# Performance work log

Hardware: AMD Instinct MI355X
Metric: run time of the kernel (lower is better)

The kernel has to match this reference:

```python
import jax, jax.numpy as jnp
import numpy as np

C_IN = 1024
C_INTER = 512  # in_channels // 2, canonical NONLocalBlock default
N_CLASSES = 13


def setup_inputs() -> dict:
    key = jax.random.key(0)
    ks = jax.random.split(key, 11)
    B, T, H, W = 16, 8, 14, 14
    s = 0.02
    return {
        "x": jax.random.normal(ks[0], (B, C_IN, T, H, W), dtype=jnp.float32),
        # 1x1x1 conv projections stored as [out, in] matrices + biases
        "g_w": jax.random.normal(ks[1], (C_INTER, C_IN), dtype=jnp.float32) * s,
        "g_b": jnp.zeros((C_INTER,), dtype=jnp.float32),
        "theta_w": jax.random.normal(ks[2], (C_INTER, C_IN), dtype=jnp.float32) * s,
        "theta_b": jnp.zeros((C_INTER,), dtype=jnp.float32),
        "phi_w": jax.random.normal(ks[3], (C_INTER, C_IN), dtype=jnp.float32) * s,
        "phi_b": jnp.zeros((C_INTER,), dtype=jnp.float32),
        "w_w": jax.random.normal(ks[4], (C_IN, C_INTER), dtype=jnp.float32) * s,
        "w_b": jnp.zeros((C_IN,), dtype=jnp.float32),
        "fc_w": jax.random.normal(ks[5], (N_CLASSES, C_IN), dtype=jnp.float32) * s,
        "fc_b": jnp.zeros((N_CLASSES,), dtype=jnp.float32),
    }


def reference(x, g_w, g_b, theta_w, theta_b, phi_w, phi_b, w_w, w_b, fc_w, fc_b):
    B, C, T, H, W = x.shape
    xf = x.reshape(B, C, -1)  # [B, C, N], N = T*H*W
    # 1x1x1 conv projections == channel matmuls
    g = jnp.einsum('oc,bcn->bno', g_w, xf) + g_b        # [B, N, 512]
    th = jnp.einsum('oc,bcn->bno', theta_w, xf) + theta_b  # [B, N, 512]
    ph = jnp.einsum('oc,bcn->bno', phi_w, xf) + phi_b      # [B, N, 512]
    # pairwise affinity (embedded Gaussian): [B, N, N]
    f = jnp.einsum('bnd,bmd->bnm', th, ph)
    attn = jax.nn.softmax(f, axis=-1)
    y = jnp.einsum('bnm,bmd->bnd', attn, g)             # [B, N, 512]
    wy = jnp.einsum('cd,bnd->bcn', w_w, y) + w_b[None, :, None]  # [B, C, N]
    z = wy.reshape(B, C, T, H, W) + x                    # residual
    pooled = z.mean(axis=(2, 3, 4))                      # adaptive avgpool (1,1,1)
    return pooled @ fc_w.T + fc_b                        # [B, 13]
```

## Files before the change

### kernel.cpp

```cpp
#include <hip/hip_runtime.h>
#include <hip/hip_bf16.h>


#define BATCH 16
#define CIN   1024
#define CINT  512
#define NSP   1568
#define NPAD  1664
#define NTIL  13
#define NCLS  13

using bf16 = __hip_bfloat16;
typedef __attribute__((ext_vector_type(8))) short short8;
typedef __attribute__((ext_vector_type(4))) float f32x4;

#define DEVI static __device__ __forceinline__

DEVI void gload16(const void* g, void* l) {
  __builtin_amdgcn_global_load_lds((const __attribute__((address_space(1))) void*)g,
                                   (__attribute__((address_space(3))) void*)l, 16, 0, 0);
}

DEVI float wave_sum(float v) {
#pragma unroll
  for (int m = 32; m; m >>= 1) v += __shfl_xor(v, m);
  return v;
}

DEVI short f2bf(float f) {
  union { __hip_bfloat16 h; short s; } u;
  u.h = __float2bfloat16(f);
  return u.s;
}

__global__ __launch_bounds__(256) void k_transpose(const float* __restrict__ x,
                                                   bf16* __restrict__ xt,
                                                   float* __restrict__ xbar) {
  __shared__ float t[128 * 37];
  const int b = blockIdx.z;
  const int n0 = blockIdx.x * 32;
  const int c0 = blockIdx.y * 128;
  const int tid = threadIdx.x;
  const int lane = tid & 63;
  const float* xb = x + (size_t)b * CIN * NSP;
  const bool pad = (n0 >= NSP);
#pragma unroll
  for (int it = 0; it < 4; ++it) {
    const int slot = it * 256 + tid;
    const int cr = slot >> 3;
    const int q = slot & 7;
    float4 v = {0.f, 0.f, 0.f, 0.f};
    if (!pad) v = *(const float4*)(xb + (size_t)(c0 + cr) * NSP + n0 + q * 4);
    t[cr * 37 + q * 4 + 0] = v.x;
    t[cr * 37 + q * 4 + 1] = v.y;
    t[cr * 37 + q * 4 + 2] = v.z;
    t[cr * 37 + q * 4 + 3] = v.w;
    float s = v.x + v.y + v.z + v.w;
    s += __shfl_xor(s, 1);
    s += __shfl_xor(s, 2);
    s += __shfl_xor(s, 4);
    if ((lane & 7) == 0 && !pad)
      atomicAdd(&xbar[b * CIN + c0 + cr], s * (1.0f / NSP));
  }
  __syncthreads();
  bf16* xo = xt + (size_t)b * NPAD * CIN;
#pragma unroll
  for (int it = 0; it < 2; ++it) {
    const int slot = it * 256 + tid;
    const int n = slot >> 4;
    const int seg = slot & 15;
    short8 o;
#pragma unroll
    for (int k = 0; k < 8; ++k) o[k] = f2bf(t[(seg * 8 + k) * 37 + n]);
    *(short8*)(xo + (size_t)(n0 + n) * CIN + c0 + seg * 8) = o;
  }
}

__global__ void k_wconv(const float* __restrict__ thw, const float* __restrict__ phw,
                        bf16* __restrict__ wb) {
  const int i4 = (blockIdx.x * 256 + threadIdx.x) * 4;
  const float* s = (i4 < 512 * 1024) ? (thw + i4) : (phw + (i4 - 512 * 1024));
  const float4 v = *(const float4*)s;
  wb[i4 + 0] = __float2bfloat16(v.x);
  wb[i4 + 1] = __float2bfloat16(v.y);
  wb[i4 + 2] = __float2bfloat16(v.z);
  wb[i4 + 3] = __float2bfloat16(v.w);
}

template <int LDK>
DEVI void gemm128_bt(const bf16* Ag, const bf16* Bg, bf16* lds,
                     f32x4 acc[4][4]) {
  const int tid = threadIdx.x;
  const int lane = tid & 63;
  const int w = tid >> 6;
  const int wr = (w >> 1) * 64;
  const int wc = (w & 1) * 64;
  const int kc_src8 = ((lane & 3) ^ ((lane >> 3) & 3)) * 8;
  const int kc_rd8 = (((lane >> 4) ^ ((lane >> 1) & 3))) * 8;
  constexpr int NT = LDK / 32;

  auto STAGE = [&](int buf, int ks) {
    bf16* lA = lds + buf * 8192;
    bf16* lB = lA + 4096;
#pragma unroll
    for (int it = 0; it < 2; ++it) {
      const int ch = w * 64 + it * 256 + lane;
      const int row = ch >> 2;
      const int lbase = (w * 64 + it * 256) * 8;
      gload16(Ag + (size_t)row * LDK + ks * 32 + kc_src8, lA + lbase);
      gload16(Bg + (size_t)row * LDK + ks * 32 + kc_src8, lB + lbase);
    }
  };
  auto COMPUTE = [&](int buf) {
    const bf16* lA = lds + buf * 8192;
    const bf16* lB = lA + 4096;
    short8 af[4], bfr[4];
#pragma unroll
    for (int i = 0; i < 4; ++i)
      af[i] = *(const short8*)(lA + (wr + i * 16 + (lane & 15)) * 32 + kc_rd8);
#pragma unroll
    for (int i = 0; i < 4; ++i)
      bfr[i] = *(const short8*)(lB + (wc + i * 16 + (lane & 15)) * 32 + kc_rd8);
#pragma unroll
    for (int m = 0; m < 4; ++m)
#pragma unroll
      for (int n = 0; n < 4; ++n)
        acc[m][n] = __builtin_amdgcn_mfma_f32_16x16x32_bf16(af[m], bfr[n], acc[m][n], 0, 0, 0);
  };

  STAGE(0, 0);
  __syncthreads();
  int ks = 0;
#pragma unroll 1
  while (ks < NT - 2) {
    STAGE(1, ks + 1);
    COMPUTE(0);
    __syncthreads();
    STAGE(0, ks + 2);
    COMPUTE(1);
    __syncthreads();
    ks += 2;
  }
  STAGE(1, NT - 1);
  COMPUTE(0);
  __syncthreads();
  COMPUTE(1);
}

__global__ __launch_bounds__(256) void k_proj(const bf16* __restrict__ xt,
                                              const bf16* __restrict__ wb,
                                              const float* __restrict__ thb,
                                              const float* __restrict__ phb,
                                              bf16* __restrict__ th,
                                              bf16* __restrict__ ph) {
  __shared__ bf16 smem[16384];
  const int id = blockIdx.x;
  const int rcls = id & 7;
  const int q = id >> 3;
  const int bm = (q >> 3) * 8 + rcls;
  const int bo = q & 7;

  f32x4 acc[4][4];
  const f32x4 z = {0.f, 0.f, 0.f, 0.f};
#pragma unroll
  for (int m = 0; m < 4; ++m)
#pragma unroll
    for (int n = 0; n < 4; ++n) acc[m][n] = z;

  gemm128_bt<CIN>(xt + (size_t)bm * 128 * CIN, wb + (size_t)bo * 128 * CIN,
                  smem, acc);

  const int tid = threadIdx.x;
  const int lane = tid & 63;
  const int w = tid >> 6;
  const int wc = (w & 1) * 64;
  const int hsel = w >> 1;
  const float* bias = (bo < 4) ? thb : phb;
  bf16* outb = (bo < 4) ? th : ph;
  const int obase = (bo & 3) * 128;
#pragma unroll
  for (int h = 0; h < 2; ++h) {
    __syncthreads();
    if (hsel == h) {
#pragma unroll
      for (int m = 0; m < 4; ++m)
#pragma unroll
        for (int n = 0; n < 4; ++n) {
          const int col_l = wc + n * 16 + (lane & 15);
          const float bv = bias[obase + col_l];
#pragma unroll
          for (int j = 0; j < 4; ++j) {
            const int lr = m * 16 + (lane >> 4) * 4 + j;
            smem[lr * 128 + (col_l ^ ((lr & 7) << 3))] =
                __float2bfloat16(acc[m][n][j] + bv);
          }
        }
    }
    __syncthreads();
#pragma unroll
    for (int it = 0; it < 4; ++it) {
      const int slot = it * 256 + tid;
      const int rr = slot >> 4;
      const int seg = slot & 15;
      const short8 v = *(const short8*)(smem + rr * 128 + ((seg ^ (rr & 7)) << 3));
      *(short8*)(outb + (size_t)(bm * 128 + h * 64 + rr) * CINT + obase + seg * 8) = v;
    }
  }
}

__global__ __launch_bounds__(256) void k_fgemm(const bf16* __restrict__ th,
                                               const bf16* __restrict__ ph,
                                               bf16* __restrict__ eb,
                                               float* __restrict__ psum) {
  __shared__ bf16 smem[16384];
  __shared__ float rsum2[2][128];
  const int id = blockIdx.x;
  const int rcls = id & 7;
  const int q = id >> 3;
  const int bloc = q / 169;
  const int t = q - bloc * 169;
  const int b = bloc * 8 + rcls;
  const int bm = t / 13;
  const int bn = t - bm * 13;

  f32x4 acc[4][4];
  const f32x4 z = {0.f, 0.f, 0.f, 0.f};
#pragma unroll
  for (int m = 0; m < 4; ++m)
#pragma unroll
    for (int n = 0; n < 4; ++n) acc[m][n] = z;

  gemm128_bt<CINT>(th + ((size_t)b * NPAD + bm * 128) * CINT,
                   ph + ((size_t)b * NPAD + bn * 128) * CINT,
                   smem, acc);

  const int tid = threadIdx.x;
  const int lane = tid & 63;
  const int w = tid >> 6;
  const int wc = (w & 1) * 64;
  const int hsel = w >> 1;
  bf16* ebb = eb + ((size_t)b * NPAD + bm * 128) * NPAD + bn * 128;
#pragma unroll
  for (int h = 0; h < 2; ++h) {
    __syncthreads();
    if (hsel == h) {
#pragma unroll
      for (int m = 0; m < 4; ++m)
#pragma unroll
        for (int j = 0; j < 4; ++j) {
          const int lr = m * 16 + (lane >> 4) * 4 + j;
          float ps = 0.f;
#pragma unroll
          for (int n = 0; n < 4; ++n) {
            const int col_l = wc + n * 16 + (lane & 15);
            const float ev = __expf(acc[m][n][j]);
            smem[lr * 128 + (col_l ^ ((lr & 7) << 3))] = __float2bfloat16(ev);
            if (bn * 128 + col_l < NSP) ps += ev;
          }
          ps += __shfl_xor(ps, 1);
          ps += __shfl_xor(ps, 2);
          ps += __shfl_xor(ps, 4);
          ps += __shfl_xor(ps, 8);
          if ((lane & 15) == 0) rsum2[w & 1][h * 64 + lr] = ps;
        }
    }
    __syncthreads();
#pragma unroll
    for (int it = 0; it < 4; ++it) {
      const int slot = it * 256 + tid;
      const int rr = slot >> 4;
      const int seg = slot & 15;
      const short8 v = *(const short8*)(smem + rr * 128 + ((seg ^ (rr & 7)) << 3));
      *(short8*)(ebb + (size_t)(h * 64 + rr) * NPAD + seg * 8) = v;
    }
  }
  if (tid < 128)
    psum[((size_t)b * NTIL + bn) * NPAD + bm * 128 + tid] =
        rsum2[0][tid] + rsum2[1][tid];
}

__global__ void k_recip(const float* __restrict__ psum, float* __restrict__ rinv) {
  const int id = blockIdx.x * 256 + threadIdx.x;
  const int b = id / NSP;
  const int n = id - b * NSP;
  float s = 0.f;
#pragma unroll
  for (int t = 0; t < NTIL; ++t) s += psum[((size_t)b * NTIL + t) * NPAD + n];
  rinv[id] = 1.0f / s;
}

__global__ void k_abar(const bf16* __restrict__ eb, const float* __restrict__ rinv,
                       float* __restrict__ abar) {
  const int m = blockIdx.x * 256 + threadIdx.x;
  const int b = blockIdx.z;
  const bool act = m < NSP;
  const bf16* fb = eb + (size_t)b * NPAD * NPAD;
  const int n0 = blockIdx.y * 196;
  float local = 0.f;
  for (int n = n0; n < n0 + 196; ++n) {
    const float iS = rinv[b * NSP + n];
    if (act) local += __bfloat162float(fb[(size_t)n * NPAD + m]) * iS;
  }
  if (act) atomicAdd(&abar[b * NSP + m], local * (1.0f / NSP));
}

__global__ void k_xg(const bf16* __restrict__ xt, const float* __restrict__ abar,
                     float* __restrict__ xg) {
  const int c = blockIdx.x * 256 + threadIdx.x;
  const int b = blockIdx.z;
  const bf16* xb = xt + (size_t)b * NPAD * CIN;
  const int n0 = blockIdx.y * 196;
  float s = 0.f;
  for (int n = n0; n < n0 + 196; ++n)
    s += __bfloat162float(xb[(size_t)n * CIN + c]) * abar[b * NSP + n];
  atomicAdd(&xg[b * CIN + c], s);
}

__global__ __launch_bounds__(64) void k_ybar(const float* __restrict__ gw,
                                             const float* __restrict__ gb,
                                             const float* __restrict__ xg,
                                             float* __restrict__ syb) {
  const int d = blockIdx.x;
  const int lane = threadIdx.x;
  const float4* wr = (const float4*)(gw + (size_t)d * CIN);
  float4 wv[4];
#pragma unroll
  for (int k = 0; k < 4; ++k) wv[k] = wr[k * 64 + lane];
  const float bv = gb[d];
#pragma unroll 1
  for (int b = 0; b < BATCH; ++b) {
    const float4* xr = (const float4*)(xg + (size_t)b * CIN);
    float s = 0.f;
#pragma unroll
    for (int k = 0; k < 4; ++k) {
      const float4 xv = xr[k * 64 + lane];
      s += wv[k].x * xv.x + wv[k].y * xv.y + wv[k].z * xv.z + wv[k].w * xv.w;
    }
    s = wave_sum(s);
    if (lane == 0) syb[b * CINT + d] = s + bv;
  }
}

__global__ __launch_bounds__(64) void k_spool(const float* __restrict__ ww,
                                              const float* __restrict__ wbias,
                                              const float* __restrict__ xbar,
                                              const float* __restrict__ syb,
                                              float* __restrict__ spool) {
  const int c = blockIdx.x;
  const int lane = threadIdx.x;
  const float4* wr = (const float4*)(ww + (size_t)c * CINT);
  float4 wv[2];
#pragma unroll
  for (int k = 0; k < 2; ++k) wv[k] = wr[k * 64 + lane];
  const float bv = wbias[c];
#pragma unroll 1
  for (int b = 0; b < BATCH; ++b) {
    const float4* yr = (const float4*)(syb + (size_t)b * CINT);
    float s = 0.f;
#pragma unroll
    for (int k = 0; k < 2; ++k) {
      const float4 yv = yr[k * 64 + lane];
      s += wv[k].x * yv.x + wv[k].y * yv.y + wv[k].z * yv.z + wv[k].w * yv.w;
    }
    s = wave_sum(s);
    if (lane == 0) spool[b * CIN + c] = s + bv + xbar[b * CIN + c];
  }
}

__global__ __launch_bounds__(64) void k_out(const float* __restrict__ spool,
                                            const float* __restrict__ fcw,
                                            const float* __restrict__ fcb,
                                            float* __restrict__ out) {
  const int b = blockIdx.x;
  const int lane = threadIdx.x;
  const float4* pr = (const float4*)(spool + (size_t)b * CIN);
  float4 pv[4];
#pragma unroll
  for (int k = 0; k < 4; ++k) pv[k] = pr[k * 64 + lane];
#pragma unroll 1
  for (int cls = 0; cls < NCLS; ++cls) {
    const float4* wr = (const float4*)(fcw + (size_t)cls * CIN);
    float s = 0.f;
#pragma unroll
    for (int k = 0; k < 4; ++k) {
      const float4 wv = wr[k * 64 + lane];
      s += wv.x * pv[k].x + wv.y * pv[k].y + wv.z * pv[k].z + wv.w * pv[k].w;
    }
    s = wave_sum(s);
    if (lane == 0) out[b * NCLS + cls] = s + fcb[cls];
  }
}

extern "C" void kernel_launch(void* const* d_in, const int* in_sizes, int n_in,
                              void* d_out, int out_size, void* d_ws, size_t ws_size,
                              hipStream_t stream) {
  const float* x    = (const float*)d_in[0];
  const float* g_w  = (const float*)d_in[1];
  const float* g_b  = (const float*)d_in[2];
  const float* th_w = (const float*)d_in[3];
  const float* th_b = (const float*)d_in[4];
  const float* ph_w = (const float*)d_in[5];
  const float* ph_b = (const float*)d_in[6];
  const float* w_w  = (const float*)d_in[7];
  const float* w_b  = (const float*)d_in[8];
  const float* fc_w = (const float*)d_in[9];
  const float* fc_b = (const float*)d_in[10];
  float* out = (float*)d_out;

  char* ws = (char*)d_ws;
  size_t off = 0;
  auto carve = [&](size_t bytes) {
    void* p = ws + off;
    off = (off + bytes + 255) & ~(size_t)255;
    return p;
  };
  bf16*  xt    = (bf16*)carve((size_t)BATCH * NPAD * CIN * 2);
  bf16*  wb    = (bf16*)carve((size_t)1024 * 1024 * 2);
  bf16*  th    = (bf16*)carve((size_t)BATCH * NPAD * CINT * 2);
  bf16*  ph    = (bf16*)carve((size_t)BATCH * NPAD * CINT * 2);
  bf16*  eb    = (bf16*)carve((size_t)BATCH * NPAD * NPAD * 2);
  float* psum  = (float*)carve((size_t)BATCH * NTIL * NPAD * 4);
  float* rinv  = (float*)carve((size_t)BATCH * NSP * 4);
  float* abar  = (float*)carve((size_t)BATCH * NSP * 4);
  float* xbar  = (float*)carve((size_t)BATCH * CIN * 4);
  float* xg    = (float*)carve((size_t)BATCH * CIN * 4);
  float* syb   = (float*)carve((size_t)BATCH * CINT * 4);
  float* spool = (float*)carve((size_t)BATCH * CIN * 4);
  (void)ws_size; (void)in_sizes; (void)n_in; (void)out_size;

  hipMemsetAsync(abar, 0, (size_t)BATCH * NSP * 4, stream);
  hipMemsetAsync(xbar, 0, (size_t)BATCH * CIN * 4, stream);
  hipMemsetAsync(xg,   0, (size_t)BATCH * CIN * 4, stream);

  k_transpose<<<dim3(52, 8, 16), 256, 0, stream>>>(x, xt, xbar);
  k_wconv<<<1024, 256, 0, stream>>>(th_w, ph_w, wb);
  k_proj<<<1664, 256, 0, stream>>>(xt, wb, th_b, ph_b, th, ph);
  k_fgemm<<<2704, 256, 0, stream>>>(th, ph, eb, psum);
  k_recip<<<98, 256, 0, stream>>>(psum, rinv);
  k_abar<<<dim3(7, 8, 16), 256, 0, stream>>>(eb, rinv, abar);
  k_xg<<<dim3(4, 8, 16), 256, 0, stream>>>(xt, abar, xg);
  k_ybar<<<512, 64, 0, stream>>>(g_w, g_b, xg, syb);
  k_spool<<<1024, 64, 0, stream>>>(w_w, w_b, xbar, syb, spool);
  k_out<<<16, 64, 0, stream>>>(spool, fc_w, fc_b, out);
}
```

Measured before the change: 311.7 us.

## Enlarge projection and affinity GEMM tiles to 256x256 and vectorize abar reduction

The shared bf16 GEMM helper now computes 256x256 output tiles with 512 threads (8 waves, each holding an 8x4 grid of MFMA accumulators) instead of 128x128 with 256 threads. Both the theta/phi projection and the exp-affinity GEMM use it, so the affinity matrix is padded to 1792 and the row-sum partials drop to 7 column tiles. The larger tiles are meant to raise reuse of each LDS tile and cut global traffic and block count, at the cost of higher register and LDS pressure and more wasted padded work. Separately, k_abar now has each thread read 8 bf16 values at once along contiguous columns, replacing scalar loads.

```diff
diff --git a/kernel.cpp b/kernel.cpp
--- a/kernel.cpp
+++ b/kernel.cpp
@@ -7,7 +7,8 @@
 #define CINT  512
 #define NSP   1568
 #define NPAD  1664
-#define NTIL  13
+#define NPAD2 1792
+#define NTIL2 7
 #define NCLS  13
 
 using bf16 = __hip_bfloat16;
@@ -31,6 +32,11 @@
   union { __hip_bfloat16 h; short s; } u;
   u.h = __float2bfloat16(f);
   return u.s;
+}
+DEVI float bf2f(short s) {
+  union { float f; unsigned u; } x;
+  x.u = ((unsigned)(unsigned short)s) << 16;
+  return x.f;
 }
 
 __global__ __launch_bounds__(256) void k_transpose(const float* __restrict__ x,
@@ -88,44 +94,43 @@
 }
 
 template <int LDK>
-DEVI void gemm128_bt(const bf16* Ag, const bf16* Bg, bf16* lds,
-                     f32x4 acc[4][4]) {
+DEVI void gemm256_bt(const bf16* Ag, const bf16* Bg, bf16* lds,
+                     f32x4 acc[8][4]) {
   const int tid = threadIdx.x;
   const int lane = tid & 63;
   const int w = tid >> 6;
-  const int wr = (w >> 1) * 64;
-  const int wc = (w & 1) * 64;
+  const int wr = (w >> 2) * 128;
+  const int wc = (w & 3) * 64;
   const int kc_src8 = ((lane & 3) ^ ((lane >> 3) & 3)) * 8;
-  const int kc_rd8 = (((lane >> 4) ^ ((lane >> 1) & 3))) * 8;
+  const int kc_rd8 = ((lane >> 4) ^ ((lane >> 1) & 3)) * 8;
   constexpr int NT = LDK / 32;
 
   auto STAGE = [&](int buf, int ks) {
-    bf16* lA = lds + buf * 8192;
-    bf16* lB = lA + 4096;
+    bf16* lA = lds + buf * 16384;
+    bf16* lB = lA + 8192;
 #pragma unroll
     for (int it = 0; it < 2; ++it) {
-      const int ch = w * 64 + it * 256 + lane;
-      const int row = ch >> 2;
-      const int lbase = (w * 64 + it * 256) * 8;
+      const int c = it * 512 + w * 64 + lane;
+      const int row = c >> 2;
+      const int lbase = (it * 512 + w * 64) * 8;
       gload16(Ag + (size_t)row * LDK + ks * 32 + kc_src8, lA + lbase);
       gload16(Bg + (size_t)row * LDK + ks * 32 + kc_src8, lB + lbase);
     }
   };
   auto COMPUTE = [&](int buf) {
-    const bf16* lA = lds + buf * 8192;
-    const bf16* lB = lA + 4096;
-    short8 af[4], bfr[4];
-#pragma unroll
-    for (int i = 0; i < 4; ++i)
-      af[i] = *(const short8*)(lA + (wr + i * 16 + (lane & 15)) * 32 + kc_rd8);
+    const bf16* lA = lds + buf * 16384;
+    const bf16* lB = lA + 8192;
+    short8 bfr[4];
 #pragma unroll
     for (int i = 0; i < 4; ++i)
       bfr[i] = *(const short8*)(lB + (wc + i * 16 + (lane & 15)) * 32 + kc_rd8);
 #pragma unroll
-    for (int m = 0; m < 4; ++m)
+    for (int m = 0; m < 8; ++m) {
+      const short8 af = *(const short8*)(lA + (wr + m * 16 + (lane & 15)) * 32 + kc_rd8);
 #pragma unroll
       for (int n = 0; n < 4; ++n)
-        acc[m][n] = __builtin_amdgcn_mfma_f32_16x16x32_bf16(af[m], bfr[n], acc[m][n], 0, 0, 0);
+        acc[m][n] = __builtin_amdgcn_mfma_f32_16x16x32_bf16(af, bfr[n], acc[m][n], 0, 0, 0);
+    }
   };
 
   STAGE(0, 0);
@@ -147,136 +152,141 @@
   COMPUTE(1);
 }
 
-__global__ __launch_bounds__(256) void k_proj(const bf16* __restrict__ xt,
-                                              const bf16* __restrict__ wb,
-                                              const float* __restrict__ thb,
-                                              const float* __restrict__ phb,
-                                              bf16* __restrict__ th,
-                                              bf16* __restrict__ ph) {
-  __shared__ bf16 smem[16384];
+__global__ __launch_bounds__(512, 2) void k_proj(const bf16* __restrict__ xt,
+                                                 const bf16* __restrict__ wb,
+                                                 const float* __restrict__ thb,
+                                                 const float* __restrict__ phb,
+                                                 bf16* __restrict__ th,
+                                                 bf16* __restrict__ ph) {
+  __shared__ bf16 smem[32768];
   const int id = blockIdx.x;
   const int rcls = id & 7;
   const int q = id >> 3;
-  const int bm = (q >> 3) * 8 + rcls;
-  const int bo = q & 7;
-
-  f32x4 acc[4][4];
+  const int bm = (q >> 2) * 8 + rcls;
+  const int bo = q & 3;
+
+  f32x4 acc[8][4];
   const f32x4 z = {0.f, 0.f, 0.f, 0.f};
 #pragma unroll
-  for (int m = 0; m < 4; ++m)
+  for (int m = 0; m < 8; ++m)
 #pragma unroll
     for (int n = 0; n < 4; ++n) acc[m][n] = z;
 
-  gemm128_bt<CIN>(xt + (size_t)bm * 128 * CIN, wb + (size_t)bo * 128 * CIN,
+  gemm256_bt<CIN>(xt + (size_t)bm * 256 * CIN, wb + (size_t)bo * 256 * CIN,
                   smem, acc);
 
   const int tid = threadIdx.x;
   const int lane = tid & 63;
   const int w = tid >> 6;
-  const int wc = (w & 1) * 64;
-  const int hsel = w >> 1;
-  const float* bias = (bo < 4) ? thb : phb;
-  bf16* outb = (bo < 4) ? th : ph;
-  const int obase = (bo & 3) * 128;
-#pragma unroll
-  for (int h = 0; h < 2; ++h) {
-    __syncthreads();
-    if (hsel == h) {
-#pragma unroll
-      for (int m = 0; m < 4; ++m)
+  const int wc = (w & 3) * 64;
+  const int wrsel = w >> 2;
+  const float* bias = (bo < 2) ? thb : phb;
+  bf16* outb = (bo < 2) ? th : ph;
+  const int obase = (bo & 1) * 256;
+#pragma unroll
+  for (int h = 0; h < 4; ++h) {
+    __syncthreads();
+    if (wrsel == (h >> 1)) {
+#pragma unroll
+      for (int mm = 0; mm < 4; ++mm) {
+        const int m = (h & 1) * 4 + mm;
 #pragma unroll
         for (int n = 0; n < 4; ++n) {
-          const int col_l = wc + n * 16 + (lane & 15);
-          const float bv = bias[obase + col_l];
+          const int col = wc + n * 16 + (lane & 15);
+          const float bv = bias[obase + col];
 #pragma unroll
           for (int j = 0; j < 4; ++j) {
-            const int lr = m * 16 + (lane >> 4) * 4 + j;
-            smem[lr * 128 + (col_l ^ ((lr & 7) << 3))] =
+            const int lr = mm * 16 + (lane >> 4) * 4 + j;
+            smem[lr * 256 + (col ^ ((lr & 7) << 3))] =
                 __float2bfloat16(acc[m][n][j] + bv);
           }
         }
+      }
     }
     __syncthreads();
 #pragma unroll
     for (int it = 0; it < 4; ++it) {
-      const int slot = it * 256 + tid;
-      const int rr = slot >> 4;
-      const int seg = slot & 15;
-      const short8 v = *(const short8*)(smem + rr * 128 + ((seg ^ (rr & 7)) << 3));
-      *(short8*)(outb + (size_t)(bm * 128 + h * 64 + rr) * CINT + obase + seg * 8) = v;
-    }
-  }
-}
-
-__global__ __launch_bounds__(256) void k_fgemm(const bf16* __restrict__ th,
-                                               const bf16* __restrict__ ph,
-                                               bf16* __restrict__ eb,
-                                               float* __restrict__ psum) {
-  __shared__ bf16 smem[16384];
-  __shared__ float rsum2[2][128];
+      const int slot = it * 512 + tid;
+      const int r = slot >> 5;
+      const int seg = slot & 31;
+      const short8 v = *(const short8*)(smem + r * 256 + ((seg ^ (r & 7)) << 3));
+      *(short8*)(outb + (size_t)(bm * 256 + h * 64 + r) * CINT + obase + seg * 8) = v;
+    }
+  }
+}
+
+__global__ __launch_bounds__(512, 2) void k_fgemm(const bf16* __restrict__ th,
+                                                  const bf16* __restrict__ ph,
+                                                  bf16* __restrict__ eb,
+                                                  float* __restrict__ psum) {
+  __shared__ bf16 smem[32768];
+  __shared__ float rsumq[4][64];
   const int id = blockIdx.x;
   const int rcls = id & 7;
   const int q = id >> 3;
-  const int bloc = q / 169;
-  const int t = q - bloc * 169;
+  const int bloc = q / 49;
+  const int t = q - bloc * 49;
   const int b = bloc * 8 + rcls;
-  const int bm = t / 13;
-  const int bn = t - bm * 13;
-
-  f32x4 acc[4][4];
+  const int bm = t / 7;
+  const int bn = t - bm * 7;
+
+  f32x4 acc[8][4];
   const f32x4 z = {0.f, 0.f, 0.f, 0.f};
 #pragma unroll
-  for (int m = 0; m < 4; ++m)
+  for (int m = 0; m < 8; ++m)
 #pragma unroll
     for (int n = 0; n < 4; ++n) acc[m][n] = z;
 
-  gemm128_bt<CINT>(th + ((size_t)b * NPAD + bm * 128) * CINT,
-                   ph + ((size_t)b * NPAD + bn * 128) * CINT,
+  gemm256_bt<CINT>(th + ((size_t)b * NPAD + bm * 256) * CINT,
+                   ph + ((size_t)b * NPAD + bn * 256) * CINT,
                    smem, acc);
 
   const int tid = threadIdx.x;
   const int lane = tid & 63;
   const int w = tid >> 6;
-  const int wc = (w & 1) * 64;
-  const int hsel = w >> 1;
-  bf16* ebb = eb + ((size_t)b * NPAD + bm * 128) * NPAD + bn * 128;
-#pragma unroll
-  for (int h = 0; h < 2; ++h) {
-    __syncthreads();
-    if (hsel == h) {
-#pragma unroll
-      for (int m = 0; m < 4; ++m)
+  const int wc = (w & 3) * 64;
+  const int wcid = w & 3;
+  const int wrsel = w >> 2;
+  bf16* ebb = eb + ((size_t)b * NPAD2 + bm * 256) * NPAD2 + bn * 256;
+#pragma unroll
+  for (int h = 0; h < 4; ++h) {
+    __syncthreads();
+    if (wrsel == (h >> 1)) {
+#pragma unroll
+      for (int mm = 0; mm < 4; ++mm) {
+        const int m = (h & 1) * 4 + mm;
 #pragma unroll
         for (int j = 0; j < 4; ++j) {
-          const int lr = m * 16 + (lane >> 4) * 4 + j;
+          const int lr = mm * 16 + (lane >> 4) * 4 + j;
           float ps = 0.f;
 #pragma unroll
           for (int n = 0; n < 4; ++n) {
-            const int col_l = wc + n * 16 + (lane & 15);
+            const int col = wc + n * 16 + (lane & 15);
             const float ev = __expf(acc[m][n][j]);
-            smem[lr * 128 + (col_l ^ ((lr & 7) << 3))] = __float2bfloat16(ev);
-            if (bn * 128 + col_l < NSP) ps += ev;
+            smem[lr * 256 + (col ^ ((lr & 7) << 3))] = __float2bfloat16(ev);
+            if (bn * 256 + col < NSP) ps += ev;
           }
           ps += __shfl_xor(ps, 1);
           ps += __shfl_xor(ps, 2);
           ps += __shfl_xor(ps, 4);
           ps += __shfl_xor(ps, 8);
-          if ((lane & 15) == 0) rsum2[w & 1][h * 64 + lr] = ps;
+          if ((lane & 15) == 0) rsumq[wcid][lr] = ps;
         }
-    }
-    __syncthreads();
+      }
+    }
+    __syncthreads();
+    if (tid < 64)
+      psum[((size_t)b * NTIL2 + bn) * NPAD2 + bm * 256 + h * 64 + tid] =
+          rsumq[0][tid] + rsumq[1][tid] + rsumq[2][tid] + rsumq[3][tid];
 #pragma unroll
     for (int it = 0; it < 4; ++it) {
-      const int slot = it * 256 + tid;
-      const int rr = slot >> 4;
-      const int seg = slot & 15;
-      const short8 v = *(const short8*)(smem + rr * 128 + ((seg ^ (rr & 7)) << 3));
-      *(short8*)(ebb + (size_t)(h * 64 + rr) * NPAD + seg * 8) = v;
-    }
-  }
-  if (tid < 128)
-    psum[((size_t)b * NTIL + bn) * NPAD + bm * 128 + tid] =
-        rsum2[0][tid] + rsum2[1][tid];
+      const int slot = it * 512 + tid;
+      const int r = slot >> 5;
+      const int seg = slot & 31;
+      const short8 v = *(const short8*)(smem + r * 256 + ((seg ^ (r & 7)) << 3));
+      *(short8*)(ebb + (size_t)(h * 64 + r) * NPAD2 + seg * 8) = v;
+    }
+  }
 }
 
 __global__ void k_recip(const float* __restrict__ psum, float* __restrict__ rinv) {
@@ -285,23 +295,30 @@
   const int n = id - b * NSP;
   float s = 0.f;
 #pragma unroll
-  for (int t = 0; t < NTIL; ++t) s += psum[((size_t)b * NTIL + t) * NPAD + n];
+  for (int t = 0; t < NTIL2; ++t) s += psum[((size_t)b * NTIL2 + t) * NPAD2 + n];
   rinv[id] = 1.0f / s;
 }
 
 __global__ void k_abar(const bf16* __restrict__ eb, const float* __restrict__ rinv,
                        float* __restrict__ abar) {
-  const int m = blockIdx.x * 256 + threadIdx.x;
-  const int b = blockIdx.z;
-  const bool act = m < NSP;
-  const bf16* fb = eb + (size_t)b * NPAD * NPAD;
-  const int n0 = blockIdx.y * 196;
-  float local = 0.f;
-  for (int n = n0; n < n0 + 196; ++n) {
+  const int b = blockIdx.y;
+  const int n0 = blockIdx.x * 49;
+  const int m0 = threadIdx.x * 8;
+  if (m0 >= NSP) return;
+  const bf16* fb = eb + (size_t)b * NPAD2 * NPAD2;
+  float a[8];
+#pragma unroll
+  for (int k = 0; k < 8; ++k) a[k] = 0.f;
+#pragma unroll 1
+  for (int n = n0; n < n0 + 49; ++n) {
     const float iS = rinv[b * NSP + n];
-    if (act) local += __bfloat162float(fb[(size_t)n * NPAD + m]) * iS;
-  }
-  if (act) atomicAdd(&abar[b * NSP + m], local * (1.0f / NSP));
+    const short8 v = *(const short8*)(fb + (size_t)n * NPAD2 + m0);
+#pragma unroll
+    for (int k = 0; k < 8; ++k) a[k] += bf2f(v[k]) * iS;
+  }
+#pragma unroll
+  for (int k = 0; k < 8; ++k)
+    atomicAdd(&abar[b * NSP + m0 + k], a[k] * (1.0f / NSP));
 }
 
 __global__ void k_xg(const bf16* __restrict__ xt, const float* __restrict__ abar,
@@ -416,10 +433,10 @@
   };
   bf16*  xt    = (bf16*)carve((size_t)BATCH * NPAD * CIN * 2);
   bf16*  wb    = (bf16*)carve((size_t)1024 * 1024 * 2);
-  bf16*  th    = (bf16*)carve((size_t)BATCH * NPAD * CINT * 2);
-  bf16*  ph    = (bf16*)carve((size_t)BATCH * NPAD * CINT * 2);
-  bf16*  eb    = (bf16*)carve((size_t)BATCH * NPAD * NPAD * 2);
-  float* psum  = (float*)carve((size_t)BATCH * NTIL * NPAD * 4);
+  bf16*  th    = (bf16*)carve(((size_t)BATCH * NPAD + 128) * CINT * 2);
+  bf16*  ph    = (bf16*)carve(((size_t)BATCH * NPAD + 128) * CINT * 2);
+  bf16*  eb    = (bf16*)carve((size_t)BATCH * NPAD2 * NPAD2 * 2);
+  float* psum  = (float*)carve((size_t)BATCH * NTIL2 * NPAD2 * 4);
   float* rinv  = (float*)carve((size_t)BATCH * NSP * 4);
   float* abar  = (float*)carve((size_t)BATCH * NSP * 4);
   float* xbar  = (float*)carve((size_t)BATCH * CIN * 4);
@@ -434,10 +451,10 @@
 
   k_transpose<<<dim3(52, 8, 16), 256, 0, stream>>>(x, xt, xbar);
   k_wconv<<<1024, 256, 0, stream>>>(th_w, ph_w, wb);
-  k_proj<<<1664, 256, 0, stream>>>(xt, wb, th_b, ph_b, th, ph);
-  k_fgemm<<<2704, 256, 0, stream>>>(th, ph, eb, psum);
+  k_proj<<<416, 512, 0, stream>>>(xt, wb, th_b, ph_b, th, ph);
+  k_fgemm<<<784, 512, 0, stream>>>(th, ph, eb, psum);
   k_recip<<<98, 256, 0, stream>>>(psum, rinv);
-  k_abar<<<dim3(7, 8, 16), 256, 0, stream>>>(eb, rinv, abar);
+  k_abar<<<dim3(32, 16), 256, 0, stream>>>(eb, rinv, abar);
   k_xg<<<dim3(4, 8, 16), 256, 0, stream>>>(xt, abar, xg);
   k_ybar<<<512, 64, 0, stream>>>(g_w, g_b, xg, syb);
   k_spool<<<1024, 64, 0, stream>>>(w_w, w_b, xbar, syb, spool);
```

Measured after the change: 320.0 us. 2.7% more time.
